# Optimization experiments

Hardware: AMD Instinct MI355X
Metric: run time of the kernel (lower is better)

The kernel has to match this reference:

```python
import jax, jax.numpy as jnp
import numpy as np

# dims: batch, spatial H x W, channels-last
B, H, W = 16, 256, 256
CIN, COUT = 32, 32
N_MODES = (32, 32)
EM0 = N_MODES[0] // 2        # 16 (eff modes along first spatial dim)
EM1 = N_MODES[1] // 2 + 1    # 17 (eff modes along last rfft dim)
WF = W // 2 + 1              # 129 rfft bins


def setup_inputs() -> dict:
    key = jax.random.key(0)
    kx, k1r, k1i, k2r, k2i, kb = jax.random.split(key, 6)
    wshape = (CIN, COUT, EM0, EM1)
    # variance-scaling-ish scale: scale=0.5, fan_avg
    wscale = np.float32(np.sqrt(0.5 / ((CIN + COUT) / 2.0)))
    return {
        "x": jax.random.normal(kx, (B, H, W, CIN), dtype=jnp.float32),
        "w1_real": jax.random.normal(k1r, wshape, dtype=jnp.float32) * wscale,
        "w1_imag": jax.random.normal(k1i, wshape, dtype=jnp.float32) * wscale,
        "w2_real": jax.random.normal(k2r, wshape, dtype=jnp.float32) * wscale,
        "w2_imag": jax.random.normal(k2i, wshape, dtype=jnp.float32) * wscale,
        "bias": jax.random.normal(kb, (1, 1, 1, COUT), dtype=jnp.float32) * 0.1,
    }


def reference(x, w1_real, w1_imag, w2_real, w2_imag, bias):
    # forward-normalized real FFT over the two spatial axes: (B,H,WF,CIN) complex64
    x_ft = jnp.fft.rfftn(x, axes=(1, 2), norm="forward")
    w1 = w1_real + 1j * w1_imag  # corner signs=(+1,): low rows
    w2 = w2_real + 1j * w2_imag  # corner signs=(-1,): high (negative-freq) rows
    # per-corner complex mode mixing: contract input channels -> output channels
    top = jnp.einsum("bhwi,iohw->bhwo", x_ft[:, :EM0, :EM1, :], w1)
    bot = jnp.einsum("bhwi,iohw->bhwo", x_ft[:, -EM0:, :EM1, :], w2)
    out_ft = jnp.zeros((B, H, WF, COUT), dtype=jnp.complex64)
    out_ft = out_ft.at[:, :EM0, :EM1, :].set(top)
    out_ft = out_ft.at[:, -EM0:, :EM1, :].set(bot)
    y = jnp.fft.irfftn(out_ft, s=(H, W), axes=(1, 2), norm="forward")
    return y + bias
```

## Files before the change

kernel.cpp:

```cpp
#include <hip/hip_runtime.h>

#define NB 16
#define NH 256
#define EM1 17
#define TWO_PI 6.283185307179586f

typedef short short8 __attribute__((ext_vector_type(8)));
typedef float floatx4 __attribute__((ext_vector_type(4)));

__device__ __forceinline__ unsigned f2b(float x){ union{float f; unsigned u;} v; v.f=x; return v.u; }
__device__ __forceinline__ float b2f(unsigned u){ union{float f; unsigned u;} v; v.u=u; return v.f; }

__device__ __forceinline__ void cmul_upd(float& tr, float& ti, float wr, float wi) {
    float nr = tr * wr - ti * wi;
    float ni = tr * wi + ti * wr;
    tr = nr; ti = ni;
}

__global__ __launch_bounds__(256) void k0_wt(const float* __restrict__ w1r,
                                             const float* __restrict__ w1i,
                                             const float* __restrict__ w2r,
                                             const float* __restrict__ w2i,
                                             float2* __restrict__ wt) {
    __shared__ __align__(16) float l1r[2176], l1i[2176], l2r[2176], l2i[2176];
    const int t = threadIdx.x;
    const int i = blockIdx.x >> 2;
    const int oq = blockIdx.x & 3;
    const size_t off = (size_t)(i * 32 + oq * 8) * 272;
    for (int u = t; u < 544; u += 256) {
        ((float4*)l1r)[u] = ((const float4*)(w1r + off))[u];
        ((float4*)l1i)[u] = ((const float4*)(w1i + off))[u];
        ((float4*)l2r)[u] = ((const float4*)(w2r + off))[u];
        ((float4*)l2i)[u] = ((const float4*)(w2i + off))[u];
    }
    __syncthreads();
    for (int v = t; v < 4352; v += 256) {
        const int kw = v >> 8;
        const int rem = v & 255;
        const int m = rem >> 3, o8 = rem & 7;
        const int h = m & 15;
        const int lidx = o8 * 272 + h * 17 + kw;
        const float vr = (m < 16) ? l1r[lidx] : l2r[lidx];
        const float vi = (m < 16) ? l1i[lidx] : l2i[lidx];
        wt[((size_t)(kw * 32 + m) * 32 + i) * 32 + oq * 8 + o8] = make_float2(vr, vi);
    }
}

__global__ __launch_bounds__(256, 2) void k1_fwdW_mfma(const float* __restrict__ x,
                                                       float* __restrict__ Xw) {
    __shared__ __align__(16) short alds[16384];
    const int t = threadIdx.x;
    const int w = t >> 6;
    const int l = t & 63;
    const int mt = w & 1;
    const int g  = w >> 1;
    const int nn = (g == 0) ? 2 : 1;

    short8 Bh[2][8], Bl[2][8];
    const float sc = 1.0f / 65536.0f;
    #pragma unroll
    for (int u = 0; u < 2; ++u) {
        const int nt  = (g == 0) ? u : 2;
        const int n   = nt * 16 + (l & 15);
        const int kwv = n >> 1;
        const int par = n & 1;
        const bool live = (u < nn) && (n < 34);
        const float dth = (TWO_PI / 256.f) * (float)kwv;
        #pragma unroll
        for (int ks = 0; ks < 8; ++ks) {
            const int k0 = ks * 32 + (l >> 4) * 8;
            float s, c; sincosf(dth * (float)k0, &s, &c);
            float sd, cd; sincosf(dth, &sd, &cd);
            short8 vh, vl;
            #pragma unroll
            for (int j = 0; j < 8; ++j) {
                float v = live ? ((par ? -s : c) * sc) : 0.f;
                unsigned ub = f2b(v);
                short h16 = (short)(ub >> 16);
                float rres = v - b2f(ub & 0xFFFF0000u);
                short l16 = (short)(f2b(rres) >> 16);
                vh[j] = h16; vl[j] = l16;
                float ncv = c * cd - s * sd, nsv = c * sd + s * cd;
                c = ncv; s = nsv;
            }
            Bh[u][ks] = vh; Bl[u][ks] = vl;
        }
    }

    const int i   = t & 31;
    const int slot = t >> 5;
    const int i15 = i & 15, imt = i >> 4;
    const int i15l = l & 15, ql = l >> 4;

    for (int ir = 0; ir < 8; ++ir) {
        const int row = blockIdx.x * 8 + ir;
        const int b = row >> 8, y = row & 255;
        __syncthreads();
        {
            const float* rp = x + (size_t)row * 8192;
            unsigned* al32 = (unsigned*)alds;
            #pragma unroll
            for (int c = 0; c < 16; ++c) {
                const int xp = slot + (c << 3);
                float v0 = rp[xp * 64 + i];
                float v1 = rp[xp * 64 + 32 + i];
                unsigned u0 = f2b(v0), u1 = f2b(v1);
                unsigned hi = (u0 >> 16) | (u1 & 0xFFFF0000u);
                float r0 = v0 - b2f(u0 & 0xFFFF0000u);
                float r1 = v1 - b2f(u1 & 0xFFFF0000u);
                unsigned lo = (f2b(r0) >> 16) | (f2b(r1) & 0xFFFF0000u);
                const int ks = xp >> 4, q = (xp & 15) >> 2, dw = xp & 3;
                const int base = (ks * 2 + imt) * 256 + (q * 16 + i15) * 4 + dw;
                al32[base] = hi;
                al32[base + 16 * 256] = lo;
            }
        }
        __syncthreads();
        floatx4 acc0 = {0.f, 0.f, 0.f, 0.f};
        floatx4 acc1 = {0.f, 0.f, 0.f, 0.f};
        #pragma unroll
        for (int ks = 0; ks < 8; ++ks) {
            const short8 ah = *(const short8*)(alds + ((ks * 2 + mt) * 512) + l * 8);
            const short8 al = *(const short8*)(alds + ((16 + ks * 2 + mt) * 512) + l * 8);
            acc0 = __builtin_amdgcn_mfma_f32_16x16x32_bf16(ah, Bh[0][ks], acc0, 0, 0, 0);
            acc0 = __builtin_amdgcn_mfma_f32_16x16x32_bf16(ah, Bl[0][ks], acc0, 0, 0, 0);
            acc0 = __builtin_amdgcn_mfma_f32_16x16x32_bf16(al, Bh[0][ks], acc0, 0, 0, 0);
            if (nn == 2) {
                acc1 = __builtin_amdgcn_mfma_f32_16x16x32_bf16(ah, Bh[1][ks], acc1, 0, 0, 0);
                acc1 = __builtin_amdgcn_mfma_f32_16x16x32_bf16(ah, Bl[1][ks], acc1, 0, 0, 0);
                acc1 = __builtin_amdgcn_mfma_f32_16x16x32_bf16(al, Bh[1][ks], acc1, 0, 0, 0);
            }
        }
        #pragma unroll
        for (int u = 0; u < 2; ++u) {
            if (u >= nn) break;
            const int nt = (g == 0) ? u : 2;
            const int n = nt * 16 + i15l;
            if (n < 34) {
                const int kwv = n >> 1, par = n & 1;
                float* dst = Xw + (((size_t)(b * 17 + kwv) * 256 + y) * 64) + par;
                const floatx4 a = (u == 0) ? acc0 : acc1;
                #pragma unroll
                for (int r = 0; r < 4; ++r) {
                    const int ii = mt * 16 + ql * 4 + r;
                    dst[ii * 2] = a[r];
                }
            }
        }
    }
}

__global__ __launch_bounds__(512) void kmid(const float2* __restrict__ Xw,
                                            const float2* __restrict__ wt,
                                            float2* __restrict__ T) {
    __shared__ __align__(16) float2 xsh[128 * 32];
    __shared__ __align__(16) float2 xhat[32 * 32];
    __shared__ __align__(16) float2 osl[32 * 32];
    const int t = threadIdx.x;
    const int bk = blockIdx.x;
    const int b = bk / 17, kw = bk - b * 17;
    const float4* src4 = (const float4*)(Xw + (size_t)bk * 8192);

    const int m1 = t & 31, ip2 = t >> 5;
    const int kh = (m1 < 16) ? m1 : m1 - 32;
    float wc, ws; sincosf(-TWO_PI * (float)kh * (1.f / 256.f), &ws, &wc);
    float tr = 1.f, ti = 0.f;
    float a0r = 0.f, a0i = 0.f, a1r = 0.f, a1i = 0.f;
    const float* xp = (const float*)xsh + ip2 * 4;
    for (int half = 0; half < 2; ++half) {
        __syncthreads();
        #pragma unroll
        for (int q = 0; q < 4; ++q) {
            int v = q * 512 + t;
            ((float4*)xsh)[v] = src4[half * 2048 + v];
        }
        __syncthreads();
        #pragma unroll 8
        for (int yy = 0; yy < 128; ++yy) {
            float4 v = *(const float4*)(xp + yy * 64);
            a0r = fmaf(v.x, tr, a0r); a0r = fmaf(-v.y, ti, a0r);
            a0i = fmaf(v.x, ti, a0i); a0i = fmaf(v.y, tr, a0i);
            a1r = fmaf(v.z, tr, a1r); a1r = fmaf(-v.w, ti, a1r);
            a1i = fmaf(v.z, ti, a1i); a1i = fmaf(v.w, tr, a1i);
            cmul_upd(tr, ti, wc, ws);
        }
    }
    *(float4*)(xhat + m1 * 32 + ip2 * 2) = make_float4(a0r, a0i, a1r, a1i);
    __syncthreads();

    {
        const int o2 = t & 15, m = t >> 4;
        const float4* wp = (const float4*)wt + ((size_t)(kw * 32 + m) * 32) * 16 + o2;
        float ar0 = 0.f, ai0 = 0.f, ar1 = 0.f, ai1 = 0.f;
        #pragma unroll 8
        for (int ii = 0; ii < 32; ++ii) {
            float2 xv = xhat[m * 32 + ii];
            float4 wv = wp[(size_t)ii * 16];
            ar0 = fmaf(xv.x, wv.x, ar0); ar0 = fmaf(-xv.y, wv.y, ar0);
            ai0 = fmaf(xv.x, wv.y, ai0); ai0 = fmaf(xv.y, wv.x, ai0);
            ar1 = fmaf(xv.x, wv.z, ar1); ar1 = fmaf(-xv.y, wv.w, ar1);
            ai1 = fmaf(xv.x, wv.w, ai1); ai1 = fmaf(xv.y, wv.z, ai1);
        }
        *(float4*)(osl + m * 32 + o2 * 2) = make_float4(ar0, ai0, ar1, ai1);
    }
    __syncthreads();

    {
        const int y = t & 255, oh = t >> 8;
        float uc, us; sincosf(TWO_PI * (float)y * (1.f / 256.f), &us, &uc);
        float tr2 = 1.f, ti2 = 0.f;
        float ar[16], ai[16];
        #pragma unroll
        for (int o = 0; o < 16; ++o) { ar[o] = 0.f; ai[o] = 0.f; }
        for (int m = 0; m < 32; ++m) {
            if (m == 16) ti2 = -ti2;
            #pragma unroll
            for (int o2 = 0; o2 < 8; ++o2) {
                float4 v = *(const float4*)((const float*)osl + m * 64 + oh * 32 + o2 * 4);
                int o = o2 * 2;
                ar[o]   = fmaf(v.x, tr2, ar[o]);   ar[o]   = fmaf(-v.y, ti2, ar[o]);
                ai[o]   = fmaf(v.x, ti2, ai[o]);   ai[o]   = fmaf(v.y, tr2, ai[o]);
                ar[o+1] = fmaf(v.z, tr2, ar[o+1]); ar[o+1] = fmaf(-v.w, ti2, ar[o+1]);
                ai[o+1] = fmaf(v.z, ti2, ai[o+1]); ai[o+1] = fmaf(v.w, tr2, ai[o+1]);
            }
            cmul_upd(tr2, ti2, uc, us);
        }
        float2* dst = T + ((size_t)(b * 256 + y) * 17 + kw) * 32 + oh * 16;
        #pragma unroll
        for (int o2 = 0; o2 < 8; ++o2)
            *(float4*)(dst + o2 * 2) =
                make_float4(ar[o2*2], ai[o2*2], ar[o2*2+1], ai[o2*2+1]);
    }
}

__global__ __launch_bounds__(256) void k5_invW(const float2* __restrict__ T,
                                               const float* __restrict__ bias,
                                               float* __restrict__ out) {
    __shared__ __align__(16) float2 tl[544];
    __shared__ float bl[32];
    const int t = threadIdx.x;
    const int blk = blockIdx.x;
    const float4* src4 = (const float4*)(T + (size_t)blk * 544);
    for (int u = t; u < 272; u += 256) ((float4*)tl)[u] = src4[u];
    if (t < 32) bl[t] = bias[t];
    __syncthreads();
    const int o8 = t & 3, xq = t >> 2;
    float c0, s0; sincosf(TWO_PI * (float)(xq * 4) * (1.f / 256.f), &s0, &c0);
    const float CC = 0.99969881869620422f, SS = 0.02454122852291229f;
    float ur[4], ui[4];
    ur[0] = c0; ui[0] = s0;
    #pragma unroll
    for (int k = 1; k < 4; ++k) {
        ur[k] = ur[k-1] * CC - ui[k-1] * SS;
        ui[k] = ur[k-1] * SS + ui[k-1] * CC;
    }
    float tr_[4], ti_[4];
    #pragma unroll
    for (int k = 0; k < 4; ++k) { tr_[k] = ur[k]; ti_[k] = ui[k]; }
    float acc[4][8];
    #pragma unroll
    for (int k = 0; k < 4; ++k)
        #pragma unroll
        for (int o = 0; o < 8; ++o) acc[k][o] = 0.f;
    #pragma unroll 4
    for (int kw = 1; kw < 17; ++kw) {
        #pragma unroll
        for (int o2 = 0; o2 < 4; ++o2) {
            float4 v = *(const float4*)((const float*)tl + kw * 64 + o8 * 16 + o2 * 4);
            #pragma unroll
            for (int k = 0; k < 4; ++k) {
                acc[k][o2*2]   = fmaf(v.x, tr_[k], acc[k][o2*2]);
                acc[k][o2*2]   = fmaf(-v.y, ti_[k], acc[k][o2*2]);
                acc[k][o2*2+1] = fmaf(v.z, tr_[k], acc[k][o2*2+1]);
                acc[k][o2*2+1] = fmaf(-v.w, ti_[k], acc[k][o2*2+1]);
            }
        }
        #pragma unroll
        for (int k = 0; k < 4; ++k) cmul_upd(tr_[k], ti_[k], ur[k], ui[k]);
    }
    float base[8];
    #pragma unroll
    for (int o = 0; o < 8; ++o) {
        int og = o8 * 8 + o;
        base[o] = tl[og].x + bl[og];
    }
    float* orow = out + (size_t)blk * 8192;
    #pragma unroll
    for (int k = 0; k < 4; ++k) {
        int xx = xq * 4 + k;
        float res[8];
        #pragma unroll
        for (int o = 0; o < 8; ++o) res[o] = fmaf(2.f, acc[k][o], base[o]);
        float* dst = orow + xx * 32 + o8 * 8;
        *(float4*)(dst)     = make_float4(res[0], res[1], res[2], res[3]);
        *(float4*)(dst + 4) = make_float4(res[4], res[5], res[6], res[7]);
    }
}

extern "C" void kernel_launch(void* const* d_in, const int* in_sizes, int n_in,
                              void* d_out, int out_size, void* d_ws, size_t ws_size,
                              hipStream_t stream) {
    const float* x    = (const float*)d_in[0];
    const float* w1r  = (const float*)d_in[1];
    const float* w1i  = (const float*)d_in[2];
    const float* w2r  = (const float*)d_in[3];
    const float* w2i  = (const float*)d_in[4];
    const float* bias = (const float*)d_in[5];
    float* out = (float*)d_out;

    char* ws = (char*)d_ws;
    float2* Xw = (float2*)ws;
    float2* T  = (float2*)(ws + 17825792);
    float2* wt = (float2*)(ws + 2 * 17825792);

    k0_wt<<<128, 256, 0, stream>>>(w1r, w1i, w2r, w2i, wt);
    k1_fwdW_mfma<<<512, 256, 0, stream>>>(x, (float*)Xw);
    kmid<<<NB * EM1, 512, 0, stream>>>(Xw, wt, T);
    k5_invW<<<NB * NH, 256, 0, stream>>>(T, bias, out);
}
```

Before: 318.7 us.

## Rewrite inverse W-transform as split-bf16 MFMA GEMM with precomputed twiddle table

The final inverse real DFT along W, which was scalar FMA with recurrence-rotated twiddles, becomes a matrix multiply on bf16 MFMA instructions. Precision is kept by splitting values into hi/lo bf16 pairs and issuing three products. A new small kernel precomputes the cos/sin twiddle matrix, including the factor-2 scaling and the DC term, as A fragments in workspace. Each block converts its T row into B fragments in LDS. This adds an extra launch and conversion work and changes rounding behaviour. Output stores become scalar strided writes rather than float4.

Measured after the change: 311.5 us. -2.2%, faster.

```diff
diff --git a/kernel.cpp b/kernel.cpp
--- a/kernel.cpp
+++ b/kernel.cpp
@@ -46,6 +46,32 @@
     }
 }
 
+__global__ __launch_bounds__(256) void k5pre(short8* __restrict__ Atab) {
+    const int c = blockIdx.x * 256 + threadIdx.x;
+    if (c >= 2048) return;
+    const int mt = c >> 7, ks = (c >> 6) & 1, l = c & 63;
+    const int x = mt * 16 + (l & 15);
+    const int kbase = ks * 32 + (l >> 4) * 8;
+    short8 vh, vl;
+    #pragma unroll
+    for (int j = 0; j < 8; ++j) {
+        const int k = kbase + j;
+        float v = 0.f;
+        if (k < 34) {
+            const int kw = k >> 1;
+            float s, ct; sincosf((TWO_PI / 256.f) * (float)(kw * x), &s, &ct);
+            const float sc2 = (kw == 0) ? 1.f : 2.f;
+            v = (k & 1) ? (-s * sc2) : (ct * sc2);
+        }
+        unsigned ub = f2b(v);
+        vh[j] = (short)(ub >> 16);
+        float r = v - b2f(ub & 0xFFFF0000u);
+        vl[j] = (short)(f2b(r) >> 16);
+    }
+    Atab[((mt * 2 + ks) * 2 + 0) * 64 + l] = vh;
+    Atab[((mt * 2 + ks) * 2 + 1) * 64 + l] = vl;
+}
+
 __global__ __launch_bounds__(256, 2) void k1_fwdW_mfma(const float* __restrict__ x,
                                                        float* __restrict__ Xw) {
     __shared__ __align__(16) short alds[16384];
@@ -233,67 +259,84 @@
     }
 }
 
-__global__ __launch_bounds__(256) void k5_invW(const float2* __restrict__ T,
+__global__ __launch_bounds__(256) void k5_mfma(const float2* __restrict__ T,
+                                               const short8* __restrict__ Atab,
                                                const float* __restrict__ bias,
                                                float* __restrict__ out) {
-    __shared__ __align__(16) float2 tl[544];
+    __shared__ __align__(16) float trl[1088];
+    __shared__ __align__(16) short bfr[8192];
     __shared__ float bl[32];
     const int t = threadIdx.x;
     const int blk = blockIdx.x;
-    const float4* src4 = (const float4*)(T + (size_t)blk * 544);
-    for (int u = t; u < 272; u += 256) ((float4*)tl)[u] = src4[u];
-    if (t < 32) bl[t] = bias[t];
-    __syncthreads();
-    const int o8 = t & 3, xq = t >> 2;
-    float c0, s0; sincosf(TWO_PI * (float)(xq * 4) * (1.f / 256.f), &s0, &c0);
-    const float CC = 0.99969881869620422f, SS = 0.02454122852291229f;
-    float ur[4], ui[4];
-    ur[0] = c0; ui[0] = s0;
-    #pragma unroll
-    for (int k = 1; k < 4; ++k) {
-        ur[k] = ur[k-1] * CC - ui[k-1] * SS;
-        ui[k] = ur[k-1] * SS + ui[k-1] * CC;
-    }
-    float tr_[4], ti_[4];
-    #pragma unroll
-    for (int k = 0; k < 4; ++k) { tr_[k] = ur[k]; ti_[k] = ui[k]; }
-    float acc[4][8];
-    #pragma unroll
-    for (int k = 0; k < 4; ++k)
-        #pragma unroll
-        for (int o = 0; o < 8; ++o) acc[k][o] = 0.f;
-    #pragma unroll 4
-    for (int kw = 1; kw < 17; ++kw) {
-        #pragma unroll
-        for (int o2 = 0; o2 < 4; ++o2) {
-            float4 v = *(const float4*)((const float*)tl + kw * 64 + o8 * 16 + o2 * 4);
-            #pragma unroll
-            for (int k = 0; k < 4; ++k) {
-                acc[k][o2*2]   = fmaf(v.x, tr_[k], acc[k][o2*2]);
-                acc[k][o2*2]   = fmaf(-v.y, ti_[k], acc[k][o2*2]);
-                acc[k][o2*2+1] = fmaf(v.z, tr_[k], acc[k][o2*2+1]);
-                acc[k][o2*2+1] = fmaf(-v.w, ti_[k], acc[k][o2*2+1]);
-            }
-        }
-        #pragma unroll
-        for (int k = 0; k < 4; ++k) cmul_upd(tr_[k], ti_[k], ur[k], ui[k]);
-    }
-    float base[8];
-    #pragma unroll
-    for (int o = 0; o < 8; ++o) {
-        int og = o8 * 8 + o;
-        base[o] = tl[og].x + bl[og];
+    {
+        const float4* src4 = (const float4*)(T + (size_t)blk * 544);
+        ((float4*)trl)[t] = src4[t];
+        if (t < 16) ((float4*)trl)[256 + t] = src4[256 + t];
+        if (t < 32) bl[t] = bias[t];
+    }
+    __syncthreads();
+    {
+        const int nt = t >> 7, ks = (t >> 6) & 1, lc = t & 63;
+        const int o = nt * 16 + (lc & 15);
+        const int kbase = ks * 32 + (lc >> 4) * 8;
+        short8 vh, vl;
+        #pragma unroll
+        for (int j = 0; j < 8; ++j) {
+            const int k = kbase + j;
+            float v = (k < 34) ? trl[(k >> 1) * 64 + o * 2 + (k & 1)] : 0.f;
+            unsigned ub = f2b(v);
+            vh[j] = (short)(ub >> 16);
+            float r = v - b2f(ub & 0xFFFF0000u);
+            vl[j] = (short)(f2b(r) >> 16);
+        }
+        short8* bp = (short8*)bfr;
+        bp[((nt * 2 + ks) * 2 + 0) * 64 + lc] = vh;
+        bp[((nt * 2 + ks) * 2 + 1) * 64 + lc] = vl;
+    }
+    __syncthreads();
+    const int w = t >> 6, l = t & 63;
+    const short8* bp = (const short8*)bfr;
+    short8 B[2][2][2];
+    #pragma unroll
+    for (int nt = 0; nt < 2; ++nt)
+        #pragma unroll
+        for (int ks = 0; ks < 2; ++ks) {
+            B[nt][ks][0] = bp[((nt * 2 + ks) * 2 + 0) * 64 + l];
+            B[nt][ks][1] = bp[((nt * 2 + ks) * 2 + 1) * 64 + l];
+        }
+    floatx4 acc[4][2];
+    #pragma unroll
+    for (int mtp = 0; mtp < 4; ++mtp) {
+        acc[mtp][0] = (floatx4){0.f, 0.f, 0.f, 0.f};
+        acc[mtp][1] = (floatx4){0.f, 0.f, 0.f, 0.f};
+    }
+    #pragma unroll
+    for (int mtp = 0; mtp < 4; ++mtp) {
+        const int mt = w * 4 + mtp;
+        #pragma unroll
+        for (int ks = 0; ks < 2; ++ks) {
+            const short8 ah = Atab[((mt * 2 + ks) * 2 + 0) * 64 + l];
+            const short8 al = Atab[((mt * 2 + ks) * 2 + 1) * 64 + l];
+            #pragma unroll
+            for (int nt = 0; nt < 2; ++nt) {
+                acc[mtp][nt] = __builtin_amdgcn_mfma_f32_16x16x32_bf16(ah, B[nt][ks][0], acc[mtp][nt], 0, 0, 0);
+                acc[mtp][nt] = __builtin_amdgcn_mfma_f32_16x16x32_bf16(ah, B[nt][ks][1], acc[mtp][nt], 0, 0, 0);
+                acc[mtp][nt] = __builtin_amdgcn_mfma_f32_16x16x32_bf16(al, B[nt][ks][0], acc[mtp][nt], 0, 0, 0);
+            }
+        }
     }
     float* orow = out + (size_t)blk * 8192;
-    #pragma unroll
-    for (int k = 0; k < 4; ++k) {
-        int xx = xq * 4 + k;
-        float res[8];
-        #pragma unroll
-        for (int o = 0; o < 8; ++o) res[o] = fmaf(2.f, acc[k][o], base[o]);
-        float* dst = orow + xx * 32 + o8 * 8;
-        *(float4*)(dst)     = make_float4(res[0], res[1], res[2], res[3]);
-        *(float4*)(dst + 4) = make_float4(res[4], res[5], res[6], res[7]);
+    const int ql = l >> 4, i15 = l & 15;
+    #pragma unroll
+    for (int nt = 0; nt < 2; ++nt) {
+        const float bb = bl[nt * 16 + i15];
+        #pragma unroll
+        for (int mtp = 0; mtp < 4; ++mtp) {
+            const int xbase = (w * 4 + mtp) * 16 + ql * 4;
+            #pragma unroll
+            for (int r = 0; r < 4; ++r)
+                orow[(size_t)(xbase + r) * 32 + nt * 16 + i15] = acc[mtp][nt][r] + bb;
+        }
     }
 }
 
@@ -309,12 +352,14 @@
     float* out = (float*)d_out;
 
     char* ws = (char*)d_ws;
-    float2* Xw = (float2*)ws;
-    float2* T  = (float2*)(ws + 17825792);
-    float2* wt = (float2*)(ws + 2 * 17825792);
-
+    float2* Xw   = (float2*)ws;
+    float2* T    = (float2*)(ws + 17825792);
+    float2* wt   = (float2*)(ws + 2 * 17825792);
+    short8* Atab = (short8*)(ws + 2 * 17825792 + 4456448);
+
+    k5pre<<<8, 256, 0, stream>>>(Atab);
     k0_wt<<<128, 256, 0, stream>>>(w1r, w1i, w2r, w2i, wt);
     k1_fwdW_mfma<<<512, 256, 0, stream>>>(x, (float*)Xw);
     kmid<<<NB * EM1, 512, 0, stream>>>(Xw, wt, T);
-    k5_invW<<<NB * NH, 256, 0, stream>>>(T, bias, out);
-}
+    k5_mfma<<<NB * NH, 256, 0, stream>>>(T, Atab, bias, out);
+}
```
